# Performance work log

Hardware: AMD Instinct MI355X
Metric: run time of the kernel (lower is better)

The kernel has to match this reference:

```python
import jax, jax.numpy as jnp
import numpy as np

N, DIM, K = 65536, 256, 4096

def setup_inputs() -> dict:
    key = jax.random.key(0)
    kx, kc = jax.random.split(key)
    x = jax.random.normal(kx, (N, DIM), dtype=jnp.float32)
    codebook = jax.random.normal(kc, (K, DIM), dtype=jnp.float32) * 0.02
    return {"x": x, "codebook": codebook}

def reference(x, codebook):
    # torch.cdist(x, codebook).argmin(-1) == argmin of squared distances;
    x_sq = jnp.sum(x * x, axis=-1, keepdims=True)           # (n, 1)
    c_sq = jnp.sum(codebook * codebook, axis=-1)            # (k,)
    dots = jnp.einsum('nd,kd->nk', x, codebook)             # (n, k) GEMM
    dist_sq = x_sq - 2.0 * dots + c_sq[None, :]             # (n, k)
    indices = jnp.argmin(dist_sq, axis=-1)                  # (n,)
    quantized = jnp.take(codebook, indices, axis=0)         # (n, dim) gather
    return (quantized, indices)
```

## Files before the change

kernel.cpp:

```cpp
#include <hip/hip_runtime.h>
#include <cfloat>

typedef _Float16 half8 __attribute__((ext_vector_type(8)));
typedef float    f32x4 __attribute__((ext_vector_type(4)));

#define N_ROWS 65536
#define DIM    256
#define KCODES 4096
#define BM 128
#define BN 128
#define BK 32
#define NSLICE (DIM / BK)
#define NCHUNK (KCODES / BN)

#define WS_CSQ 0
#define WS_CH  278528
#define WS_CL  2375680

#define GLDS(g, l) __builtin_amdgcn_global_load_lds(                       \
    (const __attribute__((address_space(1))) unsigned int*)(g),            \
    (__attribute__((address_space(3))) unsigned int*)(l), 16, 0, 0)

__global__ void prep_codes(const float* __restrict__ cb, float* __restrict__ csq,
                           _Float16* __restrict__ ch, _Float16* __restrict__ cl) {
    __shared__ float As[32 * DIM];
    const int t = threadIdx.x;
    const int c0 = blockIdx.x * 32;
    #pragma unroll
    for (int i = 0; i < 8; ++i) {
        int r = 4 * i + (t >> 6), d4 = (t & 63) * 4;
        *(float4*)&As[r * DIM + d4] = *(const float4*)&cb[(size_t)(c0 + r) * DIM + d4];
    }
    __syncthreads();
    {
        const int r = t >> 3;
        const int k0 = (t & 7) * 32;
        const float* src = &As[r * DIM + k0];
        _Float16* dh = &ch[(size_t)(c0 + r) * DIM + k0];
        _Float16* dl = &cl[(size_t)(c0 + r) * DIM + k0];
        #pragma unroll
        for (int i = 0; i < 4; ++i) {
            half8 hv, lv;
            #pragma unroll
            for (int j = 0; j < 8; ++j) {
                float sv = src[i * 8 + j] * 64.f;
                _Float16 h = (_Float16)sv;
                hv[j] = h; lv[j] = (_Float16)(sv - (float)h);
            }
            *(half8*)(dh + i * 8) = hv;
            *(half8*)(dl + i * 8) = lv;
        }
    }
    if (t < 32) {
        const float* row = &As[t * DIM];
        float s = 0.f;
        for (int k = 0; k < DIM; ++k) s = fmaf(row[k], row[k], s);
        csq[c0 + t] = s;
    }
}

__global__ __launch_bounds__(256, 2)
void vq_mfma(const float* __restrict__ x, const float* __restrict__ cb,
             const float* __restrict__ csq,
             const _Float16* __restrict__ ch, const _Float16* __restrict__ cl,
             float* out_q, float* __restrict__ out_idx) {
    __shared__ _Float16 LDS[8 * BM * BK];
    _Float16* AhS = LDS;
    _Float16* AlS = LDS + 2 * BM * BK;
    _Float16* BhS = LDS + 4 * BM * BK;
    _Float16* BlS = LDS + 6 * BM * BK;

    const int t = threadIdx.x;
    const int lane = t & 63, wave = t >> 6;
    const int wy = wave >> 1, wx = wave & 1;
    const int m = lane & 15, q = lane >> 4;
    const int n0 = blockIdx.x * BM;
    const int swz = (q ^ (m & 3)) * 8;

    {
        float*  prepF = (float*)LDS;
        double* dtmp  = (double*)(LDS + 4 * BM * BK);
        float*  xsqS  = (float*)(LDS + 6 * BM * BK);
        char*   xqw   = (char*)out_q;
        for (int g = 0; g < 4; ++g) {
            const int r0 = g * 32;
            #pragma unroll
            for (int i = 0; i < 8; ++i) {
                int r = 4 * i + (t >> 6), d4 = (t & 63) * 4;
                *(float4*)&prepF[r * DIM + d4] =
                    *(const float4*)&x[(size_t)(n0 + r0 + r) * DIM + d4];
            }
            __syncthreads();
            {
                const int r = t >> 3;
                const int col8 = (t & 7) * 8;
                char* dst = xqw + (((size_t)(n0 + r0 + r)) << 10) + (size_t)(col8 * 2);
                const float* src = &prepF[r * DIM + col8];
                #pragma unroll
                for (int i = 0; i < 4; ++i) {
                    half8 hv, lv;
                    #pragma unroll
                    for (int j = 0; j < 8; ++j) {
                        float v = src[i * 64 + j];
                        _Float16 h = (_Float16)v;
                        hv[j] = h; lv[j] = (_Float16)(v - (float)h);
                    }
                    *(half8*)(dst + i * 128) = hv;
                    *(half8*)(dst + 512 + i * 128) = lv;
                }
            }
            if (t < 128) {
                int r = t >> 2, part = t & 3;
                const float* ap = &prepF[r * DIM + 64 * part];
                double s = 0.0;
                for (int k = 0; k < 64; ++k) { double v = (double)ap[k]; s = fma(v, v, s); }
                dtmp[t] = s;
            }
            __syncthreads();
            if (t < 32)
                xsqS[r0 + t] = (float)((dtmp[4*t] + dtmp[4*t+1]) + (dtmp[4*t+2] + dtmp[4*t+3]));
            __syncthreads();
        }
    }

    float xsq_r[16];
    {
        const float* xsqS = (const float*)(LDS + 6 * BM * BK);
        #pragma unroll
        for (int s = 0; s < 16; ++s)
            xsq_r[s] = xsqS[64 * wy + 16 * (s >> 2) + 4 * q + (s & 3)];
    }
    asm volatile("s_waitcnt vmcnt(0)" ::: "memory");
    __syncthreads();

    const int rq  = lane >> 2;
    const int gph = lane & 3;
    const int glogB = ((gph ^ (rq & 3)) << 4);
    const char* xqb = (const char*)out_q;
    const char* aBase  = xqb + (((size_t)(n0 + wave * 32 + rq)) << 10) + glogB;
    const char* bBaseH = (const char*)ch + (((size_t)(wave * 32 + rq)) << 9) + glogB;
    const char* bBaseL = (const char*)cl + (((size_t)(wave * 32 + rq)) << 9) + glogB;

#define STAGE(ck2, sl2, nb) do {                                             \
    const char* a_  = aBase  + (size_t)((sl2) * 64);                         \
    const size_t bo_ = ((size_t)(ck2) << 16) + (size_t)((sl2) * 64);         \
    const char* bh_ = bBaseH + bo_;                                          \
    const char* bl_ = bBaseL + bo_;                                          \
    _Float16* Ah_ = AhS + (nb) * (BM * BK) + wave * (32 * BK);               \
    _Float16* Al_ = AlS + (nb) * (BM * BK) + wave * (32 * BK);               \
    _Float16* Bh_ = BhS + (nb) * (BN * BK) + wave * (32 * BK);               \
    _Float16* Bl_ = BlS + (nb) * (BN * BK) + wave * (32 * BK);               \
    GLDS(a_,           Ah_);                                                 \
    GLDS(a_ + 16384,   Ah_ + 16 * BK);                                       \
    GLDS(a_ + 512,     Al_);                                                 \
    GLDS(a_ + 16896,   Al_ + 16 * BK);                                       \
    GLDS(bh_,          Bh_);                                                 \
    GLDS(bh_ + 8192,   Bh_ + 16 * BK);                                       \
    GLDS(bl_,          Bl_);                                                 \
    GLDS(bl_ + 8192,   Bl_ + 16 * BK);                                       \
} while (0)

    int aoffs[4], boffs[4];
    #pragma unroll
    for (int tr = 0; tr < 4; ++tr) aoffs[tr] = (64 * wy + 16 * tr + m) * BK + swz;
    #pragma unroll
    for (int tc = 0; tc < 4; ++tc) boffs[tc] = (64 * wx + 16 * tc + m) * BK + swz;

    float best[16]; int bidx[16];
    #pragma unroll
    for (int s = 0; s < 16; ++s) { best[s] = FLT_MAX; bidx[s] = 0; }

    STAGE(0, 0, 0);
    STAGE(0, 1, 1);
    asm volatile("s_waitcnt vmcnt(8)" ::: "memory");
    __builtin_amdgcn_s_barrier();
    __builtin_amdgcn_sched_barrier(0);

    for (int chunk = 0; chunk < NCHUNK; ++chunk) {
        const int c0 = chunk * BN;
        float csq_c[4];
        #pragma unroll
        for (int tc = 0; tc < 4; ++tc) csq_c[tc] = csq[c0 + 64 * wx + 16 * tc + m];

        f32x4 acc[4][4];
        #pragma unroll
        for (int tr = 0; tr < 4; ++tr)
            #pragma unroll
            for (int tc = 0; tc < 4; ++tc) acc[tr][tc] = (f32x4){0.f, 0.f, 0.f, 0.f};

        #pragma unroll
        for (int sl = 0; sl < NSLICE; ++sl) {
            const int cbuf = sl & 1;
            const _Float16* Ahr = AhS + cbuf * (BM * BK);
            const _Float16* Alr = AlS + cbuf * (BM * BK);
            const _Float16* Bhr = BhS + cbuf * (BN * BK);
            const _Float16* Blr = BlS + cbuf * (BN * BK);

            half8 aH[4], aL[4], bH[4], bL[4];
            #pragma unroll
            for (int tr = 0; tr < 4; ++tr) {
                aH[tr] = *(const half8*)&Ahr[aoffs[tr]];
                aL[tr] = *(const half8*)&Alr[aoffs[tr]];
            }
            #pragma unroll
            for (int tc = 0; tc < 4; ++tc) {
                bH[tc] = *(const half8*)&Bhr[boffs[tc]];
                bL[tc] = *(const half8*)&Blr[boffs[tc]];
            }

            const int sl2r = sl + 2;
            const int ck2 = chunk + (sl2r >> 3);
            const int sl2 = sl2r & 7;
            const bool stg = (ck2 < NCHUNK);
            if (stg) {
                asm volatile("s_waitcnt lgkmcnt(0)" ::: "memory");
                __builtin_amdgcn_s_barrier();
                __builtin_amdgcn_sched_barrier(0);
                STAGE(ck2, sl2, cbuf);
            }

            #pragma unroll
            for (int tc = 0; tc < 4; ++tc)
                #pragma unroll
                for (int tr = 0; tr < 4; ++tr)
                    acc[tr][tc] = __builtin_amdgcn_mfma_f32_16x16x32_f16(aH[tr], bH[tc], acc[tr][tc], 0, 0, 0);
            #pragma unroll
            for (int tc = 0; tc < 4; ++tc)
                #pragma unroll
                for (int tr = 0; tr < 4; ++tr)
                    acc[tr][tc] = __builtin_amdgcn_mfma_f32_16x16x32_f16(aH[tr], bL[tc], acc[tr][tc], 0, 0, 0);
            #pragma unroll
            for (int tc = 0; tc < 4; ++tc)
                #pragma unroll
                for (int tr = 0; tr < 4; ++tr)
                    acc[tr][tc] = __builtin_amdgcn_mfma_f32_16x16x32_f16(aL[tr], bH[tc], acc[tr][tc], 0, 0, 0);

            if (sl == NSLICE - 1) {
                #pragma unroll
                for (int tc = 0; tc < 4; ++tc) {
                    int c = c0 + 64 * wx + 16 * tc + m;
                    #pragma unroll
                    for (int tr = 0; tr < 4; ++tr) {
                        #pragma unroll
                        for (int e = 0; e < 4; ++e) {
                            float dot = acc[tr][tc][e] * 0.015625f;
                            float d = fmaf(-2.f, dot, xsq_r[tr * 4 + e]) + csq_c[tc];
                            int s = tr * 4 + e;
                            if (d < best[s]) { best[s] = d; bidx[s] = c; }
                        }
                    }
                }
            }

            if (!(chunk == NCHUNK - 1 && sl == NSLICE - 1)) {
                if (stg) asm volatile("s_waitcnt vmcnt(8)" ::: "memory");
                else     asm volatile("s_waitcnt vmcnt(0)" ::: "memory");
                __builtin_amdgcn_s_barrier();
                __builtin_amdgcn_sched_barrier(0);
            }
        }
    }

    #pragma unroll
    for (int s = 0; s < 16; ++s) {
        float v = best[s]; int idx = bidx[s];
        #pragma unroll
        for (int off = 1; off < 16; off <<= 1) {
            float v2 = __shfl_xor(v, off);
            int   i2 = __shfl_xor(idx, off);
            if (v2 < v || (v2 == v && i2 < idx)) { v = v2; idx = i2; }
        }
        best[s] = v; bidx[s] = idx;
    }
    __syncthreads();
    float* rb = (float*)BhS;
    int*   ri = (int*)BlS;
    {
        int s = m;
        int row_local = 64 * wy + 16 * (s >> 2) + 4 * q + (s & 3);
        rb[row_local * 2 + wx] = best[s];
        ri[row_local * 2 + wx] = bidx[s];
    }
    __syncthreads();
    int* widx = (int*)AhS;
    if (t < BM) {
        float d0 = rb[t * 2], d1 = rb[t * 2 + 1];
        int   i0 = ri[t * 2], i1 = ri[t * 2 + 1];
        int w = (d1 < d0 || (d1 == d0 && i1 < i0)) ? i1 : i0;
        widx[t] = w;
        out_idx[n0 + t] = (float)w;
    }
    __syncthreads();
    const int l4 = t & 63, rg = t >> 6;
    #pragma unroll 4
    for (int i = 0; i < 32; ++i) {
        int r = rg + 4 * i;
        *(float4*)&out_q[(size_t)(n0 + r) * DIM + l4 * 4] =
            *(const float4*)&cb[(size_t)widx[r] * DIM + l4 * 4];
    }
#undef STAGE
}

extern "C" void kernel_launch(void* const* d_in, const int* in_sizes, int n_in,
                              void* d_out, int out_size, void* d_ws, size_t ws_size,
                              hipStream_t stream) {
    const float* x  = (const float*)d_in[0];
    const float* cb = (const float*)d_in[1];
    float* out_q   = (float*)d_out;
    float* out_idx = (float*)d_out + (size_t)N_ROWS * DIM;

    float*    csq = (float*)((char*)d_ws + WS_CSQ);
    _Float16* ch  = (_Float16*)((char*)d_ws + WS_CH);
    _Float16* cl  = (_Float16*)((char*)d_ws + WS_CL);

    prep_codes<<<KCODES / 32, 256, 0, stream>>>(cb, csq, ch, cl);
    vq_mfma<<<N_ROWS / BM, 256, 0, stream>>>(x, cb, csq, ch, cl, out_q, out_idx);
}
```

Baseline: 565.6 us.

## Software-pipeline LDS fragment loads under MFMAs and raise wave priority

Restructures the slice loop so the fragments for the next slice are read from LDS while the last third of the current slice's MFMAs (aL x bH) runs, using register double-buffering for bH and aL. The barrier for the STAGE overwrite is now unconditional, and s_setprio brackets the MFMA groups so waves issuing matrix ops get priority. The aim is to hide LDS read latency behind matrix work. The cost is more live vector registers, which could lower occupancy, plus an extra barrier per slice.

```diff
diff --git a/kernel.cpp b/kernel.cpp
--- a/kernel.cpp
+++ b/kernel.cpp
@@ -176,6 +176,16 @@
     __builtin_amdgcn_s_barrier();
     __builtin_amdgcn_sched_barrier(0);
 
+    half8 aH[4], aL[4], bH[4], bL[4];
+    #pragma unroll
+    for (int tr = 0; tr < 4; ++tr) aH[tr] = *(const half8*)&AhS[aoffs[tr]];
+    #pragma unroll
+    for (int tc = 0; tc < 4; ++tc) bH[tc] = *(const half8*)&BhS[boffs[tc]];
+    #pragma unroll
+    for (int tc = 0; tc < 4; ++tc) bL[tc] = *(const half8*)&BlS[boffs[tc]];
+    #pragma unroll
+    for (int tr = 0; tr < 4; ++tr) aL[tr] = *(const half8*)&AlS[aoffs[tr]];
+
     for (int chunk = 0; chunk < NCHUNK; ++chunk) {
         const int c0 = chunk * BN;
         float csq_c[4];
@@ -190,35 +200,18 @@
 
         #pragma unroll
         for (int sl = 0; sl < NSLICE; ++sl) {
-            const int cbuf = sl & 1;
-            const _Float16* Ahr = AhS + cbuf * (BM * BK);
-            const _Float16* Alr = AlS + cbuf * (BM * BK);
-            const _Float16* Bhr = BhS + cbuf * (BN * BK);
-            const _Float16* Blr = BlS + cbuf * (BN * BK);
-
-            half8 aH[4], aL[4], bH[4], bL[4];
-            #pragma unroll
-            for (int tr = 0; tr < 4; ++tr) {
-                aH[tr] = *(const half8*)&Ahr[aoffs[tr]];
-                aL[tr] = *(const half8*)&Alr[aoffs[tr]];
-            }
-            #pragma unroll
-            for (int tc = 0; tc < 4; ++tc) {
-                bH[tc] = *(const half8*)&Bhr[boffs[tc]];
-                bL[tc] = *(const half8*)&Blr[boffs[tc]];
-            }
-
+            const int cbuf = sl & 1, nbuf = cbuf ^ 1;
             const int sl2r = sl + 2;
             const int ck2 = chunk + (sl2r >> 3);
             const int sl2 = sl2r & 7;
             const bool stg = (ck2 < NCHUNK);
-            if (stg) {
-                asm volatile("s_waitcnt lgkmcnt(0)" ::: "memory");
-                __builtin_amdgcn_s_barrier();
-                __builtin_amdgcn_sched_barrier(0);
-                STAGE(ck2, sl2, cbuf);
-            }
-
+
+            asm volatile("s_waitcnt lgkmcnt(0)" ::: "memory");
+            __builtin_amdgcn_s_barrier();
+            __builtin_amdgcn_sched_barrier(0);
+            if (stg) STAGE(ck2, sl2, cbuf);
+
+            __builtin_amdgcn_s_setprio(1);
             #pragma unroll
             for (int tc = 0; tc < 4; ++tc)
                 #pragma unroll
@@ -229,34 +222,57 @@
                 #pragma unroll
                 for (int tr = 0; tr < 4; ++tr)
                     acc[tr][tc] = __builtin_amdgcn_mfma_f32_16x16x32_f16(aH[tr], bL[tc], acc[tr][tc], 0, 0, 0);
-            #pragma unroll
-            for (int tc = 0; tc < 4; ++tc)
-                #pragma unroll
-                for (int tr = 0; tr < 4; ++tr)
-                    acc[tr][tc] = __builtin_amdgcn_mfma_f32_16x16x32_f16(aL[tr], bH[tc], acc[tr][tc], 0, 0, 0);
-
-            if (sl == NSLICE - 1) {
-                #pragma unroll
-                for (int tc = 0; tc < 4; ++tc) {
-                    int c = c0 + 64 * wx + 16 * tc + m;
+            __builtin_amdgcn_s_setprio(0);
+
+            if (stg) asm volatile("s_waitcnt vmcnt(8)" ::: "memory");
+            else     asm volatile("s_waitcnt vmcnt(0)" ::: "memory");
+            __builtin_amdgcn_s_barrier();
+            __builtin_amdgcn_sched_barrier(0);
+
+            {
+                const _Float16* Ahn = AhS + nbuf * (BM * BK);
+                const _Float16* Bhn = BhS + nbuf * (BN * BK);
+                const _Float16* Bln = BlS + nbuf * (BN * BK);
+                const _Float16* Aln = AlS + nbuf * (BM * BK);
+                half8 nbH[4], naL[4];
+                #pragma unroll
+                for (int tr = 0; tr < 4; ++tr) aH[tr] = *(const half8*)&Ahn[aoffs[tr]];
+                #pragma unroll
+                for (int tc = 0; tc < 4; ++tc) nbH[tc] = *(const half8*)&Bhn[boffs[tc]];
+                #pragma unroll
+                for (int tc = 0; tc < 4; ++tc) bL[tc] = *(const half8*)&Bln[boffs[tc]];
+                #pragma unroll
+                for (int tr = 0; tr < 4; ++tr) naL[tr] = *(const half8*)&Aln[aoffs[tr]];
+
+                __builtin_amdgcn_s_setprio(1);
+                #pragma unroll
+                for (int tc = 0; tc < 4; ++tc)
                     #pragma unroll
-                    for (int tr = 0; tr < 4; ++tr) {
+                    for (int tr = 0; tr < 4; ++tr)
+                        acc[tr][tc] = __builtin_amdgcn_mfma_f32_16x16x32_f16(aL[tr], bH[tc], acc[tr][tc], 0, 0, 0);
+                __builtin_amdgcn_s_setprio(0);
+
+                if (sl == NSLICE - 1) {
+                    #pragma unroll
+                    for (int tc = 0; tc < 4; ++tc) {
+                        int c = c0 + 64 * wx + 16 * tc + m;
                         #pragma unroll
-                        for (int e = 0; e < 4; ++e) {
-                            float dot = acc[tr][tc][e] * 0.015625f;
-                            float d = fmaf(-2.f, dot, xsq_r[tr * 4 + e]) + csq_c[tc];
-                            int s = tr * 4 + e;
-                            if (d < best[s]) { best[s] = d; bidx[s] = c; }
+                        for (int tr = 0; tr < 4; ++tr) {
+                            #pragma unroll
+                            for (int e = 0; e < 4; ++e) {
+                                float dot = acc[tr][tc][e] * 0.015625f;
+                                float d = fmaf(-2.f, dot, xsq_r[tr * 4 + e]) + csq_c[tc];
+                                int s = tr * 4 + e;
+                                if (d < best[s]) { best[s] = d; bidx[s] = c; }
+                            }
                         }
                     }
                 }
-            }
-
-            if (!(chunk == NCHUNK - 1 && sl == NSLICE - 1)) {
-                if (stg) asm volatile("s_waitcnt vmcnt(8)" ::: "memory");
-                else     asm volatile("s_waitcnt vmcnt(0)" ::: "memory");
-                __builtin_amdgcn_s_barrier();
-                __builtin_amdgcn_sched_barrier(0);
+
+                #pragma unroll
+                for (int tc = 0; tc < 4; ++tc) bH[tc] = nbH[tc];
+                #pragma unroll
+                for (int tr = 0; tr < 4; ++tr) aL[tr] = naL[tr];
             }
         }
     }
```

Result: slower. 705.7 us (+24.8%).

## Load x fragments straight from pre-swizzled global scratch instead of LDS staging

Applied to the files above, without the earlier changes.

The prologue now writes the hi/lo fp16 split of x into the output scratch buffer in MFMA fragment order. The main loop then loads the A operand per slice straight into registers from global memory, prefetching the next slice after the MFMAs, and no longer stages it through LDS. This roughly halves LDS use and removes the A-side LDS writes and reads plus their barriers. In exchange, each slice of every chunk re-reads A from L1/L2. The explicit vmcnt waits are dropped in favour of compiler-inserted waits, which can stall on the outstanding codebook loads.

```diff
diff --git a/kernel.cpp b/kernel.cpp
--- a/kernel.cpp
+++ b/kernel.cpp
@@ -64,11 +64,11 @@
              const float* __restrict__ csq,
              const _Float16* __restrict__ ch, const _Float16* __restrict__ cl,
              float* out_q, float* __restrict__ out_idx) {
-    __shared__ _Float16 LDS[8 * BM * BK];
-    _Float16* AhS = LDS;
-    _Float16* AlS = LDS + 2 * BM * BK;
-    _Float16* BhS = LDS + 4 * BM * BK;
-    _Float16* BlS = LDS + 6 * BM * BK;
+    __shared__ char SMEM[34 * 1024];
+    _Float16* BhS = (_Float16*)SMEM;
+    _Float16* BlS = (_Float16*)(SMEM + 16384);
+    double*   dtmp = (double*)(SMEM + 32768);
+    float*    xsqS = (float*)(SMEM + 33792);
 
     const int t = threadIdx.x;
     const int lane = t & 63, wave = t >> 6;
@@ -78,24 +78,24 @@
     const int swz = (q ^ (m & 3)) * 8;
 
     {
-        float*  prepF = (float*)LDS;
-        double* dtmp  = (double*)(LDS + 4 * BM * BK);
-        float*  xsqS  = (float*)(LDS + 6 * BM * BK);
-        char*   xqw   = (char*)out_q;
+        float* prepF = (float*)SMEM;
+        char*  xqA   = (char*)out_q + ((size_t)n0 << 10);
         for (int g = 0; g < 4; ++g) {
-            const int r0 = g * 32;
             #pragma unroll
             for (int i = 0; i < 8; ++i) {
                 int r = 4 * i + (t >> 6), d4 = (t & 63) * 4;
                 *(float4*)&prepF[r * DIM + d4] =
-                    *(const float4*)&x[(size_t)(n0 + r0 + r) * DIM + d4];
+                    *(const float4*)&x[(size_t)(n0 + g * 32 + r) * DIM + d4];
             }
             __syncthreads();
             {
-                const int r = t >> 3;
-                const int col8 = (t & 7) * 8;
-                char* dst = xqw + (((size_t)(n0 + r0 + r)) << 10) + (size_t)(col8 * 2);
-                const float* src = &prepF[r * DIM + col8];
+                const int rl   = g * 32 + (t >> 3);
+                const int g2   = rl >> 6;
+                const int tr   = (rl >> 4) & 3;
+                const int mm   = rl & 15;
+                const int qq   = t & 3;
+                const int sbase = (t >> 2) & 1;
+                const float* src = &prepF[(t >> 3) * DIM + (t & 7) * 8];
                 #pragma unroll
                 for (int i = 0; i < 4; ++i) {
                     half8 hv, lv;
@@ -105,8 +105,11 @@
                         _Float16 h = (_Float16)v;
                         hv[j] = h; lv[j] = (_Float16)(v - (float)h);
                     }
-                    *(half8*)(dst + i * 128) = hv;
-                    *(half8*)(dst + 512 + i * 128) = lv;
+                    const int s_i = sbase + 2 * i;
+                    char* dst = xqA + (size_t)(((g2 * 8 + s_i) * 8 + tr * 2) * 1024
+                                               + qq * 256 + mm * 16);
+                    *(half8*)dst          = hv;
+                    *(half8*)(dst + 1024) = lv;
                 }
             }
             if (t < 128) {
@@ -118,61 +121,61 @@
             }
             __syncthreads();
             if (t < 32)
-                xsqS[r0 + t] = (float)((dtmp[4*t] + dtmp[4*t+1]) + (dtmp[4*t+2] + dtmp[4*t+3]));
+                xsqS[g * 32 + t] = (float)((dtmp[4*t] + dtmp[4*t+1]) + (dtmp[4*t+2] + dtmp[4*t+3]));
             __syncthreads();
         }
     }
 
     float xsq_r[16];
-    {
-        const float* xsqS = (const float*)(LDS + 6 * BM * BK);
-        #pragma unroll
-        for (int s = 0; s < 16; ++s)
-            xsq_r[s] = xsqS[64 * wy + 16 * (s >> 2) + 4 * q + (s & 3)];
-    }
+    #pragma unroll
+    for (int s = 0; s < 16; ++s)
+        xsq_r[s] = xsqS[64 * wy + 16 * (s >> 2) + 4 * q + (s & 3)];
     asm volatile("s_waitcnt vmcnt(0)" ::: "memory");
     __syncthreads();
 
     const int rq  = lane >> 2;
     const int gph = lane & 3;
     const int glogB = ((gph ^ (rq & 3)) << 4);
-    const char* xqb = (const char*)out_q;
-    const char* aBase  = xqb + (((size_t)(n0 + wave * 32 + rq)) << 10) + glogB;
     const char* bBaseH = (const char*)ch + (((size_t)(wave * 32 + rq)) << 9) + glogB;
     const char* bBaseL = (const char*)cl + (((size_t)(wave * 32 + rq)) << 9) + glogB;
+    const char* ablk = (const char*)out_q + ((size_t)n0 << 10)
+                     + (size_t)wy * 65536 + (size_t)lane * 16;
 
 #define STAGE(ck2, sl2, nb) do {                                             \
-    const char* a_  = aBase  + (size_t)((sl2) * 64);                         \
     const size_t bo_ = ((size_t)(ck2) << 16) + (size_t)((sl2) * 64);         \
     const char* bh_ = bBaseH + bo_;                                          \
     const char* bl_ = bBaseL + bo_;                                          \
-    _Float16* Ah_ = AhS + (nb) * (BM * BK) + wave * (32 * BK);               \
-    _Float16* Al_ = AlS + (nb) * (BM * BK) + wave * (32 * BK);               \
-    _Float16* Bh_ = BhS + (nb) * (BN * BK) + wave * (32 * BK);               \
-    _Float16* Bl_ = BlS + (nb) * (BN * BK) + wave * (32 * BK);               \
-    GLDS(a_,           Ah_);                                                 \
-    GLDS(a_ + 16384,   Ah_ + 16 * BK);                                       \
-    GLDS(a_ + 512,     Al_);                                                 \
-    GLDS(a_ + 16896,   Al_ + 16 * BK);                                       \
+    _Float16* Bh_ = BhS + (nb) * (BM * BK) + wave * (32 * BK);               \
+    _Float16* Bl_ = BlS + (nb) * (BM * BK) + wave * (32 * BK);               \
     GLDS(bh_,          Bh_);                                                 \
     GLDS(bh_ + 8192,   Bh_ + 16 * BK);                                       \
     GLDS(bl_,          Bl_);                                                 \
     GLDS(bl_ + 8192,   Bl_ + 16 * BK);                                       \
 } while (0)
 
-    int aoffs[4], boffs[4];
-    #pragma unroll
-    for (int tr = 0; tr < 4; ++tr) aoffs[tr] = (64 * wy + 16 * tr + m) * BK + swz;
+#define ALOAD(asl) do {                                                      \
+    _Pragma("unroll")                                                        \
+    for (int tr_ = 0; tr_ < 4; ++tr_) {                                      \
+        aH[tr_] = *(const half8*)(ablk + (asl) * 8192 + tr_ * 2048);         \
+        aL[tr_] = *(const half8*)(ablk + (asl) * 8192 + tr_ * 2048 + 1024);  \
+    }                                                                        \
+} while (0)
+
+    int boffs[4];
     #pragma unroll
     for (int tc = 0; tc < 4; ++tc) boffs[tc] = (64 * wx + 16 * tc + m) * BK + swz;
 
     float best[16]; int bidx[16];
     #pragma unroll
     for (int s = 0; s < 16; ++s) { best[s] = FLT_MAX; bidx[s] = 0; }
+
+    half8 aH[4], aL[4], bH[4], bL[4];
 
     STAGE(0, 0, 0);
     STAGE(0, 1, 1);
-    asm volatile("s_waitcnt vmcnt(8)" ::: "memory");
+    __builtin_amdgcn_sched_barrier(0);
+    ALOAD(0);
+    asm volatile("s_waitcnt vmcnt(12)" ::: "memory");
     __builtin_amdgcn_s_barrier();
     __builtin_amdgcn_sched_barrier(0);
 
@@ -191,32 +194,28 @@
         #pragma unroll
         for (int sl = 0; sl < NSLICE; ++sl) {
             const int cbuf = sl & 1;
-            const _Float16* Ahr = AhS + cbuf * (BM * BK);
-            const _Float16* Alr = AlS + cbuf * (BM * BK);
-            const _Float16* Bhr = BhS + cbuf * (BN * BK);
-            const _Float16* Blr = BlS + cbuf * (BN * BK);
-
-            half8 aH[4], aL[4], bH[4], bL[4];
-            #pragma unroll
-            for (int tr = 0; tr < 4; ++tr) {
-                aH[tr] = *(const half8*)&Ahr[aoffs[tr]];
-                aL[tr] = *(const half8*)&Alr[aoffs[tr]];
-            }
-            #pragma unroll
-            for (int tc = 0; tc < 4; ++tc) {
-                bH[tc] = *(const half8*)&Bhr[boffs[tc]];
-                bL[tc] = *(const half8*)&Blr[boffs[tc]];
-            }
-
             const int sl2r = sl + 2;
             const int ck2 = chunk + (sl2r >> 3);
             const int sl2 = sl2r & 7;
             const bool stg = (ck2 < NCHUNK);
+            const bool last = (chunk == NCHUNK - 1) && (sl == NSLICE - 1);
+
+            {
+                const _Float16* Bhr = BhS + cbuf * (BM * BK);
+                const _Float16* Blr = BlS + cbuf * (BM * BK);
+                #pragma unroll
+                for (int tc = 0; tc < 4; ++tc) {
+                    bH[tc] = *(const half8*)&Bhr[boffs[tc]];
+                    bL[tc] = *(const half8*)&Blr[boffs[tc]];
+                }
+            }
+
             if (stg) {
                 asm volatile("s_waitcnt lgkmcnt(0)" ::: "memory");
                 __builtin_amdgcn_s_barrier();
                 __builtin_amdgcn_sched_barrier(0);
                 STAGE(ck2, sl2, cbuf);
+                __builtin_amdgcn_sched_barrier(0);
             }
 
             #pragma unroll
@@ -234,6 +233,8 @@
                 #pragma unroll
                 for (int tr = 0; tr < 4; ++tr)
                     acc[tr][tc] = __builtin_amdgcn_mfma_f32_16x16x32_f16(aL[tr], bH[tc], acc[tr][tc], 0, 0, 0);
+
+            if (!last) ALOAD((sl + 1) & 7);
 
             if (sl == NSLICE - 1) {
                 #pragma unroll
@@ -252,9 +253,7 @@
                 }
             }
 
-            if (!(chunk == NCHUNK - 1 && sl == NSLICE - 1)) {
-                if (stg) asm volatile("s_waitcnt vmcnt(8)" ::: "memory");
-                else     asm volatile("s_waitcnt vmcnt(0)" ::: "memory");
+            if (!last) {
                 __builtin_amdgcn_s_barrier();
                 __builtin_amdgcn_sched_barrier(0);
             }
@@ -273,8 +272,8 @@
         best[s] = v; bidx[s] = idx;
     }
     __syncthreads();
-    float* rb = (float*)BhS;
-    int*   ri = (int*)BlS;
+    float* rb = (float*)SMEM;
+    int*   ri = (int*)(SMEM + 16384);
     {
         int s = m;
         int row_local = 64 * wy + 16 * (s >> 2) + 4 * q + (s & 3);
@@ -282,7 +281,7 @@
         ri[row_local * 2 + wx] = bidx[s];
     }
     __syncthreads();
-    int* widx = (int*)AhS;
+    int* widx = (int*)(SMEM + 32768);
     if (t < BM) {
         float d0 = rb[t * 2], d1 = rb[t * 2 + 1];
         int   i0 = ri[t * 2], i1 = ri[t * 2 + 1];
@@ -299,6 +298,7 @@
             *(const float4*)&cb[(size_t)widx[r] * DIM + l4 * 4];
     }
 #undef STAGE
+#undef ALOAD
 }
 
 extern "C" void kernel_launch(void* const* d_in, const int* in_sizes, int n_in,
```

After: 777.2 us. +37.4%, slower.
